# Performance work log

Measured on AMD Instinct MI355X. Metric: run time of the kernel, lower is better.

## Reference

```python
import jax, jax.numpy as jnp
import numpy as np

N_NODES = 40000
N_EDGES = 640000
D_IN = 128
D_OUT = 128


def setup_inputs() -> dict:
    key = jax.random.key(0)
    k_feat, k_src, k_dst, k_ws, k_wn = jax.random.split(key, 5)
    feat = jax.random.normal(k_feat, (N_NODES, D_IN), dtype=jnp.float32)
    src = jax.random.randint(k_src, (N_EDGES,), 0, N_NODES, dtype=jnp.int32)
    dst = jax.random.randint(k_dst, (N_EDGES,), 0, N_NODES, dtype=jnp.int32)
    # Glorot-ish init for the two dense layers
    scale = 1.0 / np.sqrt(D_IN)
    W_self = jax.random.normal(k_ws, (D_IN, D_OUT), dtype=jnp.float32) * scale
    W_neigh = jax.random.normal(k_wn, (D_IN, D_OUT), dtype=jnp.float32) * scale
    b_self = jnp.zeros((D_OUT,), dtype=jnp.float32)
    b_neigh = jnp.zeros((D_OUT,), dtype=jnp.float32)
    return {"feat": feat, "src": src, "dst": dst,
            "W_self": W_self, "b_self": b_self,
            "W_neigh": W_neigh, "b_neigh": b_neigh}


def reference(feat, src, dst, W_self, b_self, W_neigh, b_neigh):
    # --- mean aggregation: copy_src('h','m') + mean('m','neigh') ---
    # Gather source features along edges, segment-sum into dst, divide by in-degree.
    msgs = feat[src]  # [E, D_in]
    neigh_sum = jax.ops.segment_sum(msgs, dst, num_segments=N_NODES)  # [N, D_in]
    deg = jax.ops.segment_sum(jnp.ones((src.shape[0],), feat.dtype), dst,
                              num_segments=N_NODES)  # [N]
    # DGL mean reducer yields 0 for nodes with no incoming edges.
    h_neigh = neigh_sum / jnp.maximum(deg, 1.0)[:, None]
    # --- fc_self(h_self) + fc_neigh(h_neigh) ---
    rst = (feat @ W_self + b_self) + (h_neigh @ W_neigh + b_neigh)
    return rst
```

## Files before the change

kernel.cpp:

```cpp
#include <hip/hip_runtime.h>
#include <cstddef>

constexpr int NN  = 40000;
constexpr int NE  = 640000;
constexpr int DIM = 128;
constexpr int CAP = 48;
constexpr int PLANE = NN * 64;

typedef __attribute__((ext_vector_type(8))) short short8;
typedef __attribute__((ext_vector_type(4))) float floatx4;

__device__ __forceinline__ unsigned short f2bf(float x) {
    union { float f; unsigned int i; } v; v.f = x;
    unsigned int u = v.i;
    return (unsigned short)((u + 0x7fffu + ((u >> 16) & 1u)) >> 16);
}
__device__ __forceinline__ float bflo2f(unsigned int u) {
    union { unsigned int i; float f; } v; v.i = u << 16; return v.f;
}
__device__ __forceinline__ float bfhi2f(unsigned int u) {
    union { unsigned int i; float f; } v; v.i = u & 0xffff0000u; return v.f;
}

__global__ __launch_bounds__(256) void k_prep(
    const float* __restrict__ feat, const float* __restrict__ Wself,
    const float* __restrict__ Wneigh, unsigned short* __restrict__ featb,
    unsigned short* __restrict__ Wc, int* __restrict__ cnt)
{
    int b = blockIdx.x, t = threadIdx.x;
    if (b < 2500) {
        int idx8 = b * 256 + t;
        int n  = idx8 >> 4;
        int d0 = (idx8 & 15) << 3;
        const float4* fp =
            reinterpret_cast<const float4*>(feat + (size_t)n * DIM + d0);
        float4 v0 = fp[0], v1 = fp[1];
        unsigned int p0 = (unsigned int)f2bf(v0.x) | ((unsigned int)f2bf(v0.y) << 16);
        unsigned int p1 = (unsigned int)f2bf(v0.z) | ((unsigned int)f2bf(v0.w) << 16);
        unsigned int p2 = (unsigned int)f2bf(v1.x) | ((unsigned int)f2bf(v1.y) << 16);
        unsigned int p3 = (unsigned int)f2bf(v1.z) | ((unsigned int)f2bf(v1.w) << 16);
        int plane = d0 >> 6, off = d0 & 63;
        *reinterpret_cast<uint4*>(
            featb + (size_t)plane * PLANE + (size_t)n * 64 + off) =
            make_uint4(p0, p1, p2, p3);
    } else if (b < 2628) {
        int idx = (b - 2500) * 256 + t;
        int c = idx >> 13, n = (idx >> 6) & 127, kp = idx & 63;
        int k = c * 64 + kp;
        float w = (k < DIM) ? Wself[(size_t)k * DIM + n]
                            : Wneigh[(size_t)(k - DIM) * DIM + n];
        Wc[idx] = f2bf(w);
    } else {
        int i = (b - 2628) * 256 + t;
        if (i < NN) cnt[i] = 0;
    }
}

__global__ __launch_bounds__(256) void k_fill(
    const int* __restrict__ src, const int* __restrict__ dst,
    int* __restrict__ cnt, unsigned short* __restrict__ colf)
{
    int t0 = blockIdx.x * 256 + threadIdx.x;
    int d[4], s[4], pos[4];
    #pragma unroll
    for (int k = 0; k < 4; ++k) {
        int e = t0 + k * 160000;
        d[k] = dst[e];
        s[k] = src[e];
    }
    #pragma unroll
    for (int k = 0; k < 4; ++k)
        pos[k] = atomicAdd(&cnt[d[k]], 1);
    #pragma unroll
    for (int k = 0; k < 4; ++k)
        if (pos[k] < CAP) colf[d[k] * CAP + pos[k]] = (unsigned short)s[k];
}

__global__ __launch_bounds__(256) void k_gather(
    const unsigned int* __restrict__ fb32,
    const int* __restrict__ cnt,
    const unsigned short* __restrict__ colf,
    unsigned int* __restrict__ hnb32)
{
    int gtid = blockIdx.x * blockDim.x + threadIdx.x;
    int n = gtid >> 6;
    if (n >= NN) return;
    int lane = threadIdx.x & 63;

    int deg = cnt[n];
    int m = min(deg, CAP);
    int sv = (lane < m) ? (int)colf[n * CAP + lane] : 0;

    int vb = (lane >> 5) * (NN * 32) + (lane & 31);
    float ax0 = 0.f, ay0 = 0.f, ax1 = 0.f, ay1 = 0.f;
    int i = 0;
    for (; i + 7 < m; i += 8) {
        int s0 = __shfl(sv, i),     s1 = __shfl(sv, i + 1);
        int s2 = __shfl(sv, i + 2), s3 = __shfl(sv, i + 3);
        int s4 = __shfl(sv, i + 4), s5 = __shfl(sv, i + 5);
        int s6 = __shfl(sv, i + 6), s7 = __shfl(sv, i + 7);
        unsigned int u0 = fb32[vb + s0 * 32];
        unsigned int u1 = fb32[vb + s1 * 32];
        unsigned int u2 = fb32[vb + s2 * 32];
        unsigned int u3 = fb32[vb + s3 * 32];
        unsigned int u4 = fb32[vb + s4 * 32];
        unsigned int u5 = fb32[vb + s5 * 32];
        unsigned int u6 = fb32[vb + s6 * 32];
        unsigned int u7 = fb32[vb + s7 * 32];
        ax0 += bflo2f(u0); ay0 += bfhi2f(u0);
        ax1 += bflo2f(u1); ay1 += bfhi2f(u1);
        ax0 += bflo2f(u2); ay0 += bfhi2f(u2);
        ax1 += bflo2f(u3); ay1 += bfhi2f(u3);
        ax0 += bflo2f(u4); ay0 += bfhi2f(u4);
        ax1 += bflo2f(u5); ay1 += bfhi2f(u5);
        ax0 += bflo2f(u6); ay0 += bfhi2f(u6);
        ax1 += bflo2f(u7); ay1 += bfhi2f(u7);
    }
    for (; i + 3 < m; i += 4) {
        int s0 = __shfl(sv, i),     s1 = __shfl(sv, i + 1);
        int s2 = __shfl(sv, i + 2), s3 = __shfl(sv, i + 3);
        unsigned int u0 = fb32[vb + s0 * 32];
        unsigned int u1 = fb32[vb + s1 * 32];
        unsigned int u2 = fb32[vb + s2 * 32];
        unsigned int u3 = fb32[vb + s3 * 32];
        ax0 += bflo2f(u0); ay0 += bfhi2f(u0);
        ax1 += bflo2f(u1); ay1 += bfhi2f(u1);
        ax0 += bflo2f(u2); ay0 += bfhi2f(u2);
        ax1 += bflo2f(u3); ay1 += bfhi2f(u3);
    }
    for (; i < m; ++i) {
        int s0 = __shfl(sv, i);
        unsigned int u0 = fb32[vb + s0 * 32];
        ax0 += bflo2f(u0); ay0 += bfhi2f(u0);
    }
    float inv = 1.0f / fmaxf((float)deg, 1.0f);
    float ax = (ax0 + ax1) * inv, ay = (ay0 + ay1) * inv;
    hnb32[vb + n * 32] = (unsigned int)f2bf(ax) | ((unsigned int)f2bf(ay) << 16);
}

__global__ __launch_bounds__(320) void k_gemm(
    const unsigned short* __restrict__ featb,
    const unsigned short* __restrict__ hnb,
    const unsigned short* __restrict__ Wc,
    const float* __restrict__ bself, const float* __restrict__ bneigh,
    float* __restrict__ out)
{
    __shared__ unsigned short As[160 * 64];
    __shared__ unsigned short Bs[128 * 64];

    int t = threadIdx.x;
    int w = t >> 6;
    int lane = t & 63;
    int base_m = blockIdx.x * 160;

    floatx4 acc[2][8];
    #pragma unroll
    for (int a = 0; a < 2; ++a)
        #pragma unroll
        for (int b = 0; b < 8; ++b) acc[a][b] = (floatx4)0.f;

    for (int c = 0; c < 4; ++c) {
        const unsigned short* srcp =
            ((c < 2) ? featb + (size_t)c * PLANE
                     : hnb + (size_t)(c - 2) * PLANE) + (size_t)base_m * 64;
        #pragma unroll
        for (int it = 0; it < 4; ++it) {
            int slot = t + it * 320;
            __builtin_amdgcn_global_load_lds(
                (const __attribute__((address_space(1))) unsigned int*)(srcp + slot * 8),
                (__attribute__((address_space(3))) unsigned int*)(As + slot * 8),
                16, 0, 0);
        }
        if (t < 256) {
            const unsigned short* bp = Wc + (size_t)c * 128 * 64;
            #pragma unroll
            for (int it = 0; it < 4; ++it) {
                int slot = t + it * 256;
                __builtin_amdgcn_global_load_lds(
                    (const __attribute__((address_space(1))) unsigned int*)(bp + slot * 8),
                    (__attribute__((address_space(3))) unsigned int*)(Bs + slot * 8),
                    16, 0, 0);
            }
        }
        __syncthreads();

        #pragma unroll
        for (int s = 0; s < 2; ++s) {
            int koff = s * 32 + (lane >> 4) * 8;
            short8 af[2];
            #pragma unroll
            for (int mt = 0; mt < 2; ++mt) {
                int m = w * 32 + mt * 16 + (lane & 15);
                af[mt] = *reinterpret_cast<const short8*>(As + m * 64 + koff);
            }
            #pragma unroll
            for (int nt = 0; nt < 8; ++nt) {
                int n = nt * 16 + (lane & 15);
                short8 bf = *reinterpret_cast<const short8*>(Bs + n * 64 + koff);
                acc[0][nt] = __builtin_amdgcn_mfma_f32_16x16x32_bf16(
                    af[0], bf, acc[0][nt], 0, 0, 0);
                acc[1][nt] = __builtin_amdgcn_mfma_f32_16x16x32_bf16(
                    af[1], bf, acc[1][nt], 0, 0, 0);
            }
        }
        __syncthreads();
    }

    int colb = lane & 15;
    int quad = lane >> 4;
    #pragma unroll
    for (int nt = 0; nt < 8; ++nt) {
        int col = nt * 16 + colb;
        float bb = bself[col] + bneigh[col];
        #pragma unroll
        for (int mt = 0; mt < 2; ++mt) {
            #pragma unroll
            for (int r = 0; r < 4; ++r) {
                int row = base_m + w * 32 + mt * 16 + quad * 4 + r;
                out[(size_t)row * DIM + col] = acc[mt][nt][r] + bb;
            }
        }
    }
}

extern "C" void kernel_launch(void* const* d_in, const int* in_sizes, int n_in,
                              void* d_out, int out_size, void* d_ws, size_t ws_size,
                              hipStream_t stream)
{
    const float* feat   = (const float*)d_in[0];
    const int*   src    = (const int*)d_in[1];
    const int*   dst    = (const int*)d_in[2];
    const float* Wself  = (const float*)d_in[3];
    const float* bself  = (const float*)d_in[4];
    const float* Wneigh = (const float*)d_in[5];
    const float* bneigh = (const float*)d_in[6];
    float* out = (float*)d_out;

    char* ws = (char*)d_ws;
    unsigned short* featb = (unsigned short*)(ws);
    unsigned short* hnb   = (unsigned short*)(ws + 10240000);
    unsigned short* colf  = (unsigned short*)(ws + 20480000);
    unsigned short* Wc    = (unsigned short*)(ws + 24320000);
    int*            cnt   = (int*)(ws + 24385536);

    k_prep<<<2785, 256, 0, stream>>>(feat, Wself, Wneigh, featb, Wc, cnt);

    k_fill<<<625, 256, 0, stream>>>(src, dst, cnt, colf);

    k_gather<<<(NN * 64) / 256, 256, 0, stream>>>(
        (const unsigned int*)featb, cnt, colf, (unsigned int*)hnb);

    k_gemm<<<NN / 160, 320, 0, stream>>>(featb, hnb, Wc, bself, bneigh, out);
}
```

Baseline: 148.8 us.

## Partition edge fill by destination range and XOR-swizzle GEMM LDS tiles

```diff
diff --git a/kernel.cpp b/kernel.cpp
--- a/kernel.cpp
+++ b/kernel.cpp
@@ -9,6 +9,7 @@
 
 typedef __attribute__((ext_vector_type(8))) short short8;
 typedef __attribute__((ext_vector_type(4))) float floatx4;
+typedef __attribute__((ext_vector_type(4))) unsigned int uint32x4;
 
 __device__ __forceinline__ unsigned short f2bf(float x) {
     union { float f; unsigned int i; } v; v.f = x;
@@ -60,20 +61,23 @@
     const int* __restrict__ src, const int* __restrict__ dst,
     int* __restrict__ cnt, unsigned short* __restrict__ colf)
 {
-    int t0 = blockIdx.x * 256 + threadIdx.x;
-    int d[4], s[4], pos[4];
-    #pragma unroll
-    for (int k = 0; k < 4; ++k) {
-        int e = t0 + k * 160000;
-        d[k] = dst[e];
-        s[k] = src[e];
-    }
-    #pragma unroll
-    for (int k = 0; k < 4; ++k)
-        pos[k] = atomicAdd(&cnt[d[k]], 1);
-    #pragma unroll
-    for (int k = 0; k < 4; ++k)
-        if (pos[k] < CAP) colf[d[k] * CAP + pos[k]] = (unsigned short)s[k];
+    int r  = blockIdx.x & 7;
+    int bi = blockIdx.x >> 3;
+    int lo = r * 5000, hi = lo + 5000;
+    const uint32x4* d4 = reinterpret_cast<const uint32x4*>(dst) + (size_t)bi * 2000;
+    const uint32x4* s4 = reinterpret_cast<const uint32x4*>(src) + (size_t)bi * 2000;
+    for (int it = threadIdx.x; it < 2000; it += 256) {
+        uint32x4 dv = __builtin_nontemporal_load(d4 + it);
+        uint32x4 sv = __builtin_nontemporal_load(s4 + it);
+        #pragma unroll
+        for (int k = 0; k < 4; ++k) {
+            int d = (int)dv[k];
+            if (d >= lo && d < hi) {
+                int pos = atomicAdd(&cnt[d], 1);
+                if (pos < CAP) colf[d * CAP + pos] = (unsigned short)sv[k];
+            }
+        }
+    }
 }
 
 __global__ __launch_bounds__(256) void k_gather(
@@ -165,38 +169,44 @@
                      : hnb + (size_t)(c - 2) * PLANE) + (size_t)base_m * 64;
         #pragma unroll
         for (int it = 0; it < 4; ++it) {
-            int slot = t + it * 320;
+            int s = t + it * 320;
+            int m = s >> 3, g = s & 7;
+            const unsigned short* sa = srcp + m * 64 + ((g ^ (m & 7)) << 3);
             __builtin_amdgcn_global_load_lds(
-                (const __attribute__((address_space(1))) unsigned int*)(srcp + slot * 8),
-                (__attribute__((address_space(3))) unsigned int*)(As + slot * 8),
+                (const __attribute__((address_space(1))) unsigned int*)sa,
+                (__attribute__((address_space(3))) unsigned int*)(As + s * 8),
                 16, 0, 0);
         }
         if (t < 256) {
             const unsigned short* bp = Wc + (size_t)c * 128 * 64;
             #pragma unroll
             for (int it = 0; it < 4; ++it) {
-                int slot = t + it * 256;
+                int s = t + it * 256;
+                int n = s >> 3, g = s & 7;
+                const unsigned short* sb = bp + n * 64 + ((g ^ (n & 7)) << 3);
                 __builtin_amdgcn_global_load_lds(
-                    (const __attribute__((address_space(1))) unsigned int*)(bp + slot * 8),
-                    (__attribute__((address_space(3))) unsigned int*)(Bs + slot * 8),
+                    (const __attribute__((address_space(1))) unsigned int*)sb,
+                    (__attribute__((address_space(3))) unsigned int*)(Bs + s * 8),
                     16, 0, 0);
             }
         }
         __syncthreads();
 
         #pragma unroll
-        for (int s = 0; s < 2; ++s) {
-            int koff = s * 32 + (lane >> 4) * 8;
+        for (int sstep = 0; sstep < 2; ++sstep) {
+            int gk = sstep * 4 + (lane >> 4);
             short8 af[2];
             #pragma unroll
             for (int mt = 0; mt < 2; ++mt) {
                 int m = w * 32 + mt * 16 + (lane & 15);
-                af[mt] = *reinterpret_cast<const short8*>(As + m * 64 + koff);
+                af[mt] = *reinterpret_cast<const short8*>(
+                    As + m * 64 + ((gk ^ (m & 7)) << 3));
             }
             #pragma unroll
             for (int nt = 0; nt < 8; ++nt) {
                 int n = nt * 16 + (lane & 15);
-                short8 bf = *reinterpret_cast<const short8*>(Bs + n * 64 + koff);
+                short8 bf = *reinterpret_cast<const short8*>(
+                    Bs + n * 64 + ((gk ^ (n & 7)) << 3));
                 acc[0][nt] = __builtin_amdgcn_mfma_f32_16x16x32_bf16(
                     af[0], bf, acc[0][nt], 0, 0, 0);
                 acc[1][nt] = __builtin_amdgcn_mfma_f32_16x16x32_bf16(
@@ -245,7 +255,7 @@
 
     k_prep<<<2785, 256, 0, stream>>>(feat, Wself, Wneigh, featb, Wc, cnt);
 
-    k_fill<<<625, 256, 0, stream>>>(src, dst, cnt, colf);
+    k_fill<<<640, 256, 0, stream>>>(src, dst, cnt, colf);
 
     k_gather<<<(NN * 64) / 256, 256, 0, stream>>>(
         (const unsigned int*)featb, cnt, colf, (unsigned int*)hnb);
```

After: 148.3 us. Within noise of the previous version (-0.4%).

## Fuse prep, fill, gather and GEMM into one persistent kernel with grid barriers

Applied to the files above, without the earlier changes.

```diff
diff --git a/kernel.cpp b/kernel.cpp
--- a/kernel.cpp
+++ b/kernel.cpp
@@ -6,6 +6,14 @@
 constexpr int DIM = 128;
 constexpr int CAP = 48;
 constexpr int PLANE = NN * 64;
+constexpr int GRID = 256;
+constexpr int BLKT = 512;
+constexpr int NTHR = GRID * BLKT;
+constexpr int NWAVE = NTHR / 64;
+
+constexpr unsigned int MG1 = 0x5a6e0001u;
+constexpr unsigned int MG2 = 0x5a6e0002u;
+constexpr unsigned int MG3 = 0x5a6e0003u;
 
 typedef __attribute__((ext_vector_type(8))) short short8;
 typedef __attribute__((ext_vector_type(4))) float floatx4;
@@ -22,14 +30,51 @@
     union { unsigned int i; float f; } v; v.i = u & 0xffff0000u; return v.f;
 }
 
-__global__ __launch_bounds__(256) void k_prep(
-    const float* __restrict__ feat, const float* __restrict__ Wself,
-    const float* __restrict__ Wneigh, unsigned short* __restrict__ featb,
-    unsigned short* __restrict__ Wc, int* __restrict__ cnt)
+__device__ __forceinline__ void gbar(unsigned int* flags, unsigned int magic) {
+    __syncthreads();
+    if (threadIdx.x == 0) {
+        __threadfence();
+        __hip_atomic_store(flags + blockIdx.x, magic,
+                           __ATOMIC_RELEASE, __HIP_MEMORY_SCOPE_AGENT);
+    }
+    if (threadIdx.x < 64) {
+        int l = threadIdx.x;
+        for (int spin = 0; spin < 2000000; ++spin) {
+            unsigned int ok = 1u;
+            #pragma unroll
+            for (int q = 0; q < 4; ++q) {
+                unsigned int v = __hip_atomic_load(
+                    flags + q * 64 + l, __ATOMIC_RELAXED,
+                    __HIP_MEMORY_SCOPE_AGENT);
+                ok &= (unsigned int)(v == magic);
+            }
+            if (__all(ok)) break;
+            __builtin_amdgcn_s_sleep(8);
+        }
+    }
+    __syncthreads();
+    __threadfence();
+}
+
+__global__ __launch_bounds__(512, 2) void k_one(
+    const float* __restrict__ feat, const int* __restrict__ src,
+    const int* __restrict__ dst, const float* __restrict__ Wself,
+    const float* __restrict__ Wneigh, const float* __restrict__ bself,
+    const float* __restrict__ bneigh, unsigned short* __restrict__ featb,
+    unsigned short* __restrict__ hnb, unsigned short* __restrict__ colf,
+    unsigned short* __restrict__ Wc, int* __restrict__ cnt,
+    unsigned int* __restrict__ flags, float* __restrict__ out)
 {
+    __shared__ unsigned short As[160 * 64];
+    __shared__ unsigned short Bs[128 * 64];
+
     int b = blockIdx.x, t = threadIdx.x;
-    if (b < 2500) {
-        int idx8 = b * 256 + t;
+    int gtid = b * BLKT + t;
+    int lane = t & 63;
+
+    for (int i = gtid; i < NN; i += NTHR) cnt[i] = 0;
+
+    for (int idx8 = gtid; idx8 < NN * 16; idx8 += NTHR) {
         int n  = idx8 >> 4;
         int d0 = (idx8 & 15) << 3;
         const float4* fp =
@@ -43,181 +88,153 @@
         *reinterpret_cast<uint4*>(
             featb + (size_t)plane * PLANE + (size_t)n * 64 + off) =
             make_uint4(p0, p1, p2, p3);
-    } else if (b < 2628) {
-        int idx = (b - 2500) * 256 + t;
-        int c = idx >> 13, n = (idx >> 6) & 127, kp = idx & 63;
+    }
+
+    if (gtid < 32768) {
+        int c = gtid >> 13, n = (gtid >> 6) & 127, kp = gtid & 63;
         int k = c * 64 + kp;
         float w = (k < DIM) ? Wself[(size_t)k * DIM + n]
                             : Wneigh[(size_t)(k - DIM) * DIM + n];
-        Wc[idx] = f2bf(w);
-    } else {
-        int i = (b - 2628) * 256 + t;
-        if (i < NN) cnt[i] = 0;
-    }
-}
-
-__global__ __launch_bounds__(256) void k_fill(
-    const int* __restrict__ src, const int* __restrict__ dst,
-    int* __restrict__ cnt, unsigned short* __restrict__ colf)
-{
-    int t0 = blockIdx.x * 256 + threadIdx.x;
-    int d[4], s[4], pos[4];
-    #pragma unroll
-    for (int k = 0; k < 4; ++k) {
-        int e = t0 + k * 160000;
-        d[k] = dst[e];
-        s[k] = src[e];
-    }
-    #pragma unroll
-    for (int k = 0; k < 4; ++k)
-        pos[k] = atomicAdd(&cnt[d[k]], 1);
-    #pragma unroll
-    for (int k = 0; k < 4; ++k)
-        if (pos[k] < CAP) colf[d[k] * CAP + pos[k]] = (unsigned short)s[k];
-}
-
-__global__ __launch_bounds__(256) void k_gather(
-    const unsigned int* __restrict__ fb32,
-    const int* __restrict__ cnt,
-    const unsigned short* __restrict__ colf,
-    unsigned int* __restrict__ hnb32)
-{
-    int gtid = blockIdx.x * blockDim.x + threadIdx.x;
-    int n = gtid >> 6;
-    if (n >= NN) return;
-    int lane = threadIdx.x & 63;
-
-    int deg = cnt[n];
-    int m = min(deg, CAP);
-    int sv = (lane < m) ? (int)colf[n * CAP + lane] : 0;
-
-    int vb = (lane >> 5) * (NN * 32) + (lane & 31);
-    float ax0 = 0.f, ay0 = 0.f, ax1 = 0.f, ay1 = 0.f;
-    int i = 0;
-    for (; i + 7 < m; i += 8) {
-        int s0 = __shfl(sv, i),     s1 = __shfl(sv, i + 1);
-        int s2 = __shfl(sv, i + 2), s3 = __shfl(sv, i + 3);
-        int s4 = __shfl(sv, i + 4), s5 = __shfl(sv, i + 5);
-        int s6 = __shfl(sv, i + 6), s7 = __shfl(sv, i + 7);
-        unsigned int u0 = fb32[vb + s0 * 32];
-        unsigned int u1 = fb32[vb + s1 * 32];
-        unsigned int u2 = fb32[vb + s2 * 32];
-        unsigned int u3 = fb32[vb + s3 * 32];
-        unsigned int u4 = fb32[vb + s4 * 32];
-        unsigned int u5 = fb32[vb + s5 * 32];
-        unsigned int u6 = fb32[vb + s6 * 32];
-        unsigned int u7 = fb32[vb + s7 * 32];
-        ax0 += bflo2f(u0); ay0 += bfhi2f(u0);
-        ax1 += bflo2f(u1); ay1 += bfhi2f(u1);
-        ax0 += bflo2f(u2); ay0 += bfhi2f(u2);
-        ax1 += bflo2f(u3); ay1 += bfhi2f(u3);
-        ax0 += bflo2f(u4); ay0 += bfhi2f(u4);
-        ax1 += bflo2f(u5); ay1 += bfhi2f(u5);
-        ax0 += bflo2f(u6); ay0 += bfhi2f(u6);
-        ax1 += bflo2f(u7); ay1 += bfhi2f(u7);
-    }
-    for (; i + 3 < m; i += 4) {
-        int s0 = __shfl(sv, i),     s1 = __shfl(sv, i + 1);
-        int s2 = __shfl(sv, i + 2), s3 = __shfl(sv, i + 3);
-        unsigned int u0 = fb32[vb + s0 * 32];
-        unsigned int u1 = fb32[vb + s1 * 32];
-        unsigned int u2 = fb32[vb + s2 * 32];
-        unsigned int u3 = fb32[vb + s3 * 32];
-        ax0 += bflo2f(u0); ay0 += bfhi2f(u0);
-        ax1 += bflo2f(u1); ay1 += bfhi2f(u1);
-        ax0 += bflo2f(u2); ay0 += bfhi2f(u2);
-        ax1 += bflo2f(u3); ay1 += bfhi2f(u3);
-    }
-    for (; i < m; ++i) {
-        int s0 = __shfl(sv, i);
-        unsigned int u0 = fb32[vb + s0 * 32];
-        ax0 += bflo2f(u0); ay0 += bfhi2f(u0);
-    }
-    float inv = 1.0f / fmaxf((float)deg, 1.0f);
-    float ax = (ax0 + ax1) * inv, ay = (ay0 + ay1) * inv;
-    hnb32[vb + n * 32] = (unsigned int)f2bf(ax) | ((unsigned int)f2bf(ay) << 16);
-}
-
-__global__ __launch_bounds__(320) void k_gemm(
-    const unsigned short* __restrict__ featb,
-    const unsigned short* __restrict__ hnb,
-    const unsigned short* __restrict__ Wc,
-    const float* __restrict__ bself, const float* __restrict__ bneigh,
-    float* __restrict__ out)
-{
-    __shared__ unsigned short As[160 * 64];
-    __shared__ unsigned short Bs[128 * 64];
-
-    int t = threadIdx.x;
-    int w = t >> 6;
-    int lane = t & 63;
-    int base_m = blockIdx.x * 160;
-
-    floatx4 acc[2][8];
-    #pragma unroll
-    for (int a = 0; a < 2; ++a)
+        Wc[gtid] = f2bf(w);
+    }
+    gbar(flags, MG1);
+
+    for (int e = gtid; e < NE; e += NTHR) {
+        int d = dst[e];
+        int pos = atomicAdd(&cnt[d], 1);
+        if (pos < CAP) colf[d * CAP + pos] = (unsigned short)src[e];
+    }
+    gbar(flags, MG2);
+
+    {
+        const unsigned int* fb32 = reinterpret_cast<const unsigned int*>(featb);
+        unsigned int* hnb32 = reinterpret_cast<unsigned int*>(hnb);
+        int vb = (lane >> 5) * (NN * 32) + (lane & 31);
+        for (int n = (gtid >> 6); n < NN; n += NWAVE) {
+            int deg = cnt[n];
+            int m = min(deg, CAP);
+            int sv = (lane < m) ? (int)colf[n * CAP + lane] : 0;
+            float ax0 = 0.f, ay0 = 0.f, ax1 = 0.f, ay1 = 0.f;
+            int i = 0;
+            for (; i + 7 < m; i += 8) {
+                int s0 = __shfl(sv, i),     s1 = __shfl(sv, i + 1);
+                int s2 = __shfl(sv, i + 2), s3 = __shfl(sv, i + 3);
+                int s4 = __shfl(sv, i + 4), s5 = __shfl(sv, i + 5);
+                int s6 = __shfl(sv, i + 6), s7 = __shfl(sv, i + 7);
+                unsigned int u0 = fb32[vb + s0 * 32];
+                unsigned int u1 = fb32[vb + s1 * 32];
+                unsigned int u2 = fb32[vb + s2 * 32];
+                unsigned int u3 = fb32[vb + s3 * 32];
+                unsigned int u4 = fb32[vb + s4 * 32];
+                unsigned int u5 = fb32[vb + s5 * 32];
+                unsigned int u6 = fb32[vb + s6 * 32];
+                unsigned int u7 = fb32[vb + s7 * 32];
+                ax0 += bflo2f(u0); ay0 += bfhi2f(u0);
+                ax1 += bflo2f(u1); ay1 += bfhi2f(u1);
+                ax0 += bflo2f(u2); ay0 += bfhi2f(u2);
+                ax1 += bflo2f(u3); ay1 += bfhi2f(u3);
+                ax0 += bflo2f(u4); ay0 += bfhi2f(u4);
+                ax1 += bflo2f(u5); ay1 += bfhi2f(u5);
+                ax0 += bflo2f(u6); ay0 += bfhi2f(u6);
+                ax1 += bflo2f(u7); ay1 += bfhi2f(u7);
+            }
+            for (; i + 3 < m; i += 4) {
+                int s0 = __shfl(sv, i),     s1 = __shfl(sv, i + 1);
+                int s2 = __shfl(sv, i + 2), s3 = __shfl(sv, i + 3);
+                unsigned int u0 = fb32[vb + s0 * 32];
+                unsigned int u1 = fb32[vb + s1 * 32];
+                unsigned int u2 = fb32[vb + s2 * 32];
+                unsigned int u3 = fb32[vb + s3 * 32];
+                ax0 += bflo2f(u0); ay0 += bfhi2f(u0);
+                ax1 += bflo2f(u1); ay1 += bfhi2f(u1);
+                ax0 += bflo2f(u2); ay0 += bfhi2f(u2);
+                ax1 += bflo2f(u3); ay1 += bfhi2f(u3);
+            }
+            for (; i < m; ++i) {
+                int s0 = __shfl(sv, i);
+                unsigned int u0 = fb32[vb + s0 * 32];
+                ax0 += bflo2f(u0); ay0 += bfhi2f(u0);
+            }
+            float inv = 1.0f / fmaxf((float)deg, 1.0f);
+            float ax = (ax0 + ax1) * inv, ay = (ay0 + ay1) * inv;
+            hnb32[vb + n * 32] =
+                (unsigned int)f2bf(ax) | ((unsigned int)f2bf(ay) << 16);
+        }
+    }
+    gbar(flags, MG3);
+
+    if (b < 250) {
+        int w = t >> 6;
+        int base_m = b * 160;
+        floatx4 acc[2][8];
         #pragma unroll
-        for (int b = 0; b < 8; ++b) acc[a][b] = (floatx4)0.f;
-
-    for (int c = 0; c < 4; ++c) {
-        const unsigned short* srcp =
-            ((c < 2) ? featb + (size_t)c * PLANE
-                     : hnb + (size_t)(c - 2) * PLANE) + (size_t)base_m * 64;
-        #pragma unroll
-        for (int it = 0; it < 4; ++it) {
-            int slot = t + it * 320;
-            __builtin_amdgcn_global_load_lds(
-                (const __attribute__((address_space(1))) unsigned int*)(srcp + slot * 8),
-                (__attribute__((address_space(3))) unsigned int*)(As + slot * 8),
-                16, 0, 0);
-        }
-        if (t < 256) {
+        for (int a = 0; a < 2; ++a)
+            #pragma unroll
+            for (int q = 0; q < 8; ++q) acc[a][q] = (floatx4)0.f;
+
+        for (int c = 0; c < 4; ++c) {
+            const unsigned short* srcp =
+                ((c < 2) ? featb + (size_t)c * PLANE
+                         : hnb + (size_t)(c - 2) * PLANE) + (size_t)base_m * 64;
+            #pragma unroll
+            for (int it = 0; it < 3; ++it) {
+                int slot = t + it * 512;
+                if (slot < 1280)
+                    __builtin_amdgcn_global_load_lds(
+                        (const __attribute__((address_space(1))) unsigned int*)(srcp + slot * 8),
+                        (__attribute__((address_space(3))) unsigned int*)(As + slot * 8),
+                        16, 0, 0);
+            }
             const unsigned short* bp = Wc + (size_t)c * 128 * 64;
             #pragma unroll
-            for (int it = 0; it < 4; ++it) {
-                int slot = t + it * 256;
+            for (int it = 0; it < 2; ++it) {
+                int slot = t + it * 512;
                 __builtin_amdgcn_global_load_lds(
                     (const __attribute__((address_space(1))) unsigned int*)(bp + slot * 8),
                     (__attribute__((address_space(3))) unsigned int*)(Bs + slot * 8),
                     16, 0, 0);
             }
-        }
-        __syncthreads();
-
-        #pragma unroll
-        for (int s = 0; s < 2; ++s) {
-            int koff = s * 32 + (lane >> 4) * 8;
-            short8 af[2];
-            #pragma unroll
-            for (int mt = 0; mt < 2; ++mt) {
-                int m = w * 32 + mt * 16 + (lane & 15);
-                af[mt] = *reinterpret_cast<const short8*>(As + m * 64 + koff);
-            }
+            __syncthreads();
+
+            if (w < 5) {
+                #pragma unroll
+                for (int s = 0; s < 2; ++s) {
+                    int koff = s * 32 + (lane >> 4) * 8;
+                    short8 af[2];
+                    #pragma unroll
+                    for (int mt = 0; mt < 2; ++mt) {
+                        int m = w * 32 + mt * 16 + (lane & 15);
+                        af[mt] = *reinterpret_cast<const short8*>(As + m * 64 + koff);
+                    }
+                    #pragma unroll
+                    for (int nt = 0; nt < 8; ++nt) {
+                        int n = nt * 16 + (lane & 15);
+                        short8 bf = *reinterpret_cast<const short8*>(Bs + n * 64 + koff);
+                        acc[0][nt] = __builtin_amdgcn_mfma_f32_16x16x32_bf16(
+                            af[0], bf, acc[0][nt], 0, 0, 0);
+                        acc[1][nt] = __builtin_amdgcn_mfma_f32_16x16x32_bf16(
+                            af[1], bf, acc[1][nt], 0, 0, 0);
+                    }
+                }
+            }
+            __syncthreads();
+        }
+
+        if (w < 5) {
+            int colb = lane & 15;
+            int quad = lane >> 4;
             #pragma unroll
             for (int nt = 0; nt < 8; ++nt) {
-                int n = nt * 16 + (lane & 15);
-                short8 bf = *reinterpret_cast<const short8*>(Bs + n * 64 + koff);
-                acc[0][nt] = __builtin_amdgcn_mfma_f32_16x16x32_bf16(
-                    af[0], bf, acc[0][nt], 0, 0, 0);
-                acc[1][nt] = __builtin_amdgcn_mfma_f32_16x16x32_bf16(
-                    af[1], bf, acc[1][nt], 0, 0, 0);
-            }
-        }
-        __syncthreads();
-    }
-
-    int colb = lane & 15;
-    int quad = lane >> 4;
-    #pragma unroll
-    for (int nt = 0; nt < 8; ++nt) {
-        int col = nt * 16 + colb;
-        float bb = bself[col] + bneigh[col];
-        #pragma unroll
-        for (int mt = 0; mt < 2; ++mt) {
-            #pragma unroll
-            for (int r = 0; r < 4; ++r) {
-                int row = base_m + w * 32 + mt * 16 + quad * 4 + r;
-                out[(size_t)row * DIM + col] = acc[mt][nt][r] + bb;
+                int col = nt * 16 + colb;
+                float bb = bself[col] + bneigh[col];
+                #pragma unroll
+                for (int mt = 0; mt < 2; ++mt) {
+                    #pragma unroll
+                    for (int r = 0; r < 4; ++r) {
+                        int row = base_m + w * 32 + mt * 16 + quad * 4 + r;
+                        out[(size_t)row * DIM + col] = acc[mt][nt][r] + bb;
+                    }
+                }
             }
         }
     }
@@ -242,13 +259,9 @@
     unsigned short* colf  = (unsigned short*)(ws + 20480000);
     unsigned short* Wc    = (unsigned short*)(ws + 24320000);
     int*            cnt   = (int*)(ws + 24385536);
-
-    k_prep<<<2785, 256, 0, stream>>>(feat, Wself, Wneigh, featb, Wc, cnt);
-
-    k_fill<<<625, 256, 0, stream>>>(src, dst, cnt, colf);
-
-    k_gather<<<(NN * 64) / 256, 256, 0, stream>>>(
-        (const unsigned int*)featb, cnt, colf, (unsigned int*)hnb);
-
-    k_gemm<<<NN / 160, 320, 0, stream>>>(featb, hnb, Wc, bself, bneigh, out);
-}
+    unsigned int*   flags = (unsigned int*)(ws + 24545536);
+
+    k_one<<<GRID, BLKT, 0, stream>>>(
+        feat, src, dst, Wself, Wneigh, bself, bneigh,
+        featb, hnb, colf, Wc, cnt, flags, out);
+}
```

Measured after the change: 307.3 us. 106% more time.
